# Optimization experiments

Hardware: AMD Instinct MI355X
Metric: run time of the kernel (lower is better)

## Reference

```python
import jax, jax.numpy as jnp
from jax import lax
import numpy as np

B, T, F = 64, 128, 16
H = 512
S = 2  # num_seg; SEG_DICT['2'] = [8, 6], seg_cumsum = [2, 10, 16]


def timestep_embedding(t, dim, max_period=10000.0):
    half = dim // 2
    freqs = jnp.exp(-jnp.log(max_period) * jnp.arange(half, dtype=jnp.float32) / half)
    args = t[:, None] * freqs  # [N, half]
    return jnp.concatenate([jnp.cos(args), jnp.sin(args)], axis=-1)  # [N, dim]


def setup_inputs() -> dict:
    key = jax.random.key(0)
    ks = jax.random.split(key, 16)
    sc = lambda *sh: 1.0 / np.sqrt(sh[-1])
    inp = {
        'x': jax.random.normal(ks[0], (B, T, F), dtype=jnp.float32),
        'lengths': jax.random.randint(ks[1], (B,), 1, T + 1),
        'h0': jax.random.uniform(ks[2], (B, H), dtype=jnp.float32),
        'c0': jax.random.uniform(ks[3], (B, H), dtype=jnp.float32),
        'W_is0': jax.random.normal(ks[4], (H, 8), dtype=jnp.float32) * sc(8),
        'b_is0': jax.random.normal(ks[5], (H,), dtype=jnp.float32) * 0.01,
        'W_is1': jax.random.normal(ks[6], (H, 6), dtype=jnp.float32) * sc(6),
        'b_is1': jax.random.normal(ks[7], (H,), dtype=jnp.float32) * 0.01,
        'W_ih': jax.random.normal(ks[8], (4 * H, 3 * H), dtype=jnp.float32) * sc(3 * H),
        'W_hh': jax.random.normal(ks[9], (4 * H, H), dtype=jnp.float32) * sc(H),
        'b_ih': jax.random.normal(ks[10], (4 * H,), dtype=jnp.float32) * 0.01,
        'b_hh': jax.random.normal(ks[11], (4 * H,), dtype=jnp.float32) * 0.01,
        'W_o': jax.random.normal(ks[12], (F - 2, S * H), dtype=jnp.float32) * sc(S * H),
        'b_o': jax.random.normal(ks[13], (F - 2,), dtype=jnp.float32) * 0.01,
    }
    return inp


def reference(x, lengths, h0, c0, W_is0, b_is0, W_is1, b_is1,
              W_ih, W_hh, b_ih, b_hh, W_o, b_o):
    b, t, f = x.shape
    h = h0.shape[1]
    xf = x.reshape(-1, f)  # [B*T, F]

    # timestep embeddings from the two time columns (learning_type='diff')
    tc = timestep_embedding(xf[:, 0], h)
    tp = timestep_embedding(xf[:, 1], h)
    t_emb = jnp.concatenate([tc, tp], axis=-1)  # [B*T, 2H]

    # per-segment input linears (segments = cols 2:10 and 10:16)
    e0 = xf[:, 2:10] @ W_is0.T + b_is0
    e1 = xf[:, 10:16] @ W_is1.T + b_is1
    e0 = jnp.concatenate([e0, t_emb], axis=-1)[:, None, :]  # [B*T, 1, 3H]
    e1 = jnp.concatenate([e1, t_emb], axis=-1)[:, None, :]
    # faithful to torch: concat on dim=1 then reshape(batch, num_seg, seq_len, -1)
    embs = jnp.concatenate([e0, e1], axis=1).reshape(b, S, t, 3 * h)

    def cell(carry, xt):
        hh, cc = carry
        gates = xt @ W_ih.T + b_ih + hh @ W_hh.T + b_hh
        i, fg, g, o = jnp.split(gates, 4, axis=-1)  # torch LSTMCell order i,f,g,o
        cc = jax.nn.sigmoid(fg) * cc + jax.nn.sigmoid(i) * jnp.tanh(g)
        hh = jax.nn.sigmoid(o) * jnp.tanh(cc)
        return (hh, cc), hh

    hs = []
    for s in range(S):  # shared cell weights across segments (same nn.LSTMCell object)
        xs = jnp.swapaxes(embs[:, s], 0, 1)  # [T, B, 3H]
        _, h_seq = lax.scan(cell, (h0, c0), xs)  # [T, B, H]
        hs.append(jnp.swapaxes(h_seq, 0, 1))  # [B, T, H]
    hidden_states = jnp.stack(hs, axis=-2)  # [B, T, S, H]; dropout rate 0 -> identity

    idx = lengths - 1  # final valid timestep per sequence
    hfin = hidden_states[jnp.arange(b), idx].reshape(b, S * h)  # [B, S*H]
    out = jax.nn.sigmoid(hfin @ W_o.T + b_o)  # mlp_o: Linear + Sigmoid
    return out
```

## Files before the change

### kernel.cpp

```cpp
#include <hip/hip_runtime.h>
#include <hip/hip_bf16.h>
#include <stdint.h>


typedef __attribute__((ext_vector_type(8))) short bf16x8_t;
typedef __attribute__((ext_vector_type(4))) float f32x4_t;

#define SENT 0xAAAAAAAAu

#define OFF_G      0u
#define OFF_TEMB   33554432u
#define OFF_HH     50331648u
#define OFF_WHH    67239936u
#define OFF_WMID   69337088u
#define OFF_WC0    73531392u
#define OFF_WC1    73596928u
#define OFF_BC     73662464u
#define OFF_HFIN   73678848u
#define OFF_GFLAG  73940992u

__device__ __forceinline__ float bf2f(uint16_t u){
  union { uint32_t i; float f; } v; v.i = ((uint32_t)u) << 16; return v.f;
}
__device__ __forceinline__ uint16_t f2b(float f){
  union { float f; uint32_t i; } v; v.f = f;
  uint32_t r = v.i + 0x7fffu + ((v.i >> 16) & 1u);
  return (uint16_t)(r >> 16);
}
__device__ __forceinline__ float sigm(float x){ return 1.0f/(1.0f + __expf(-x)); }
__device__ __forceinline__ float tanh_(float x){
  float xc = fminf(fmaxf(x, -15.f), 15.f);
  float t = __expf(2.f*xc);
  return (t - 1.f)/(t + 1.f);
}
__device__ __forceinline__ void gl_lds16(const void* g, void* l){
  __builtin_amdgcn_global_load_lds(
      (const __attribute__((address_space(1))) void*)g,
      (__attribute__((address_space(3))) void*)l, 16, 0, 0);
}

__global__ void prepAll(const float* __restrict__ x,
                        const float* __restrict__ W_ih, const float* __restrict__ W_hh,
                        const float* __restrict__ W_is0, const float* __restrict__ b_is0,
                        const float* __restrict__ W_is1, const float* __restrict__ b_is1,
                        const float* __restrict__ b_ih, const float* __restrict__ b_hh,
                        const float* __restrict__ h0,
                        uint16_t* __restrict__ whh_b, uint16_t* __restrict__ wmid_b,
                        float* __restrict__ wc0, float* __restrict__ wc1,
                        float* __restrict__ bc,
                        uint16_t* __restrict__ temb, uint16_t* __restrict__ h_hist,
                        uint32_t* __restrict__ gflag){
  const int bid = blockIdx.x, tid = threadIdx.x;
  if (bid < 2048){
    const int n = bid;
    __shared__ float wrow[512];
    __shared__ float red[16][17];
    wrow[tid]       = W_ih[(size_t)n*1536 + tid];
    wrow[tid + 256] = W_ih[(size_t)n*1536 + 256 + tid];
    for (int j = tid; j < 1024; j += 256)
      wmid_b[(size_t)n*1024 + j] = f2b(W_ih[(size_t)n*1536 + 512 + j]);
    for (int k = tid; k < 512; k += 256)
      whh_b[(size_t)n*512 + k] = f2b(W_hh[(size_t)n*512 + k]);
    __syncthreads();
    {
      const int d = tid >> 4, jp = tid & 15;
      float s = 0.f;
      const int kk0 = jp*32;
      if (d < 8){
        for (int k = kk0; k < kk0 + 32; ++k) s += wrow[k]*W_is0[k*8 + d];
      } else if (d < 14){
        int c = d - 8;
        for (int k = kk0; k < kk0 + 32; ++k) s += wrow[k]*W_is1[k*6 + c];
      } else if (d == 14){
        for (int k = kk0; k < kk0 + 32; ++k) s += wrow[k]*b_is0[k];
      } else {
        for (int k = kk0; k < kk0 + 32; ++k) s += wrow[k]*b_is1[k];
      }
      red[d][jp] = s;
    }
    __syncthreads();
    if (tid < 16){
      float tot = 0.f;
      #pragma unroll
      for (int i = 0; i < 16; ++i) tot += red[tid][i];
      if (tid < 8)        wc0[n*8 + tid] = tot;
      else if (tid < 14)  wc1[n*8 + (tid - 8)] = tot;
      else if (tid == 14) bc[n]        = b_ih[n] + b_hh[n] + tot;
      else                bc[2048 + n] = b_ih[n] + b_hh[n] + tot;
    } else if (tid == 16){
      wc1[n*8 + 6] = 0.f; wc1[n*8 + 7] = 0.f;
    }
  } else if (bid < 10240){
    const int rid = bid - 2048;
    const int k = tid;
    float x0 = x[(size_t)rid*16 + 0], x1 = x[(size_t)rid*16 + 1];
    float f = __expf((float)k * (-9.210340371976184f/256.f));
    float a0 = x0*f, a1 = x1*f;
    size_t base = (size_t)rid*1024;
    temb[base + k]        = f2b(__cosf(a0));
    temb[base + 256 + k]  = f2b(__sinf(a0));
    temb[base + 512 + k]  = f2b(__cosf(a1));
    temb[base + 768 + k]  = f2b(__sinf(a1));
  } else if (bid < 10368){
    int i = (bid - 10240)*256 + tid;
    uint32_t* hh = (uint32_t*)h_hist;
    int e    = i*2;
    int rrcg = e >> 9;
    int rr   = rrcg >> 4, cg = rrcg & 15;
    int rm   = e & 511;
    int row  = rm >> 5, u = rm & 31;
    int b    = (rr*16 + row) & 63;
    int unit = cg*32 + u;
    uint32_t lo = f2b(h0[(size_t)b*512 + unit]);
    uint32_t hi = f2b(h0[(size_t)b*512 + unit + 1]);
    uint32_t wd = lo | (hi << 16);
    if (wd == SENT) wd ^= 1u;
    hh[i] = wd;
    if (i < 1024) gflag[i] = 0u;
  } else {
    uint32_t* hh = (uint32_t*)h_hist;
    size_t w0 = 32768u + ((size_t)(bid - 10368)*256 + tid)*8;
    uint4 s4 = make_uint4(SENT, SENT, SENT, SENT);
    *(uint4*)&hh[w0]     = s4;
    *(uint4*)&hh[w0 + 4] = s4;
  }
}

__launch_bounds__(256)
__global__ void fusedk(const float* __restrict__ x, const float* __restrict__ c0,
                       const int* __restrict__ lengths,
                       const uint16_t* __restrict__ whh_b, const uint16_t* __restrict__ temb,
                       const uint16_t* __restrict__ wmid,
                       const float* __restrict__ wc0, const float* __restrict__ wc1,
                       const float* __restrict__ bc,
                       uint16_t* __restrict__ G, uint16_t* __restrict__ h_hist,
                       uint32_t* __restrict__ gflag, float* __restrict__ hfin){
  __shared__ __align__(16) uint16_t smem_u[17664];
  const int tid = threadIdx.x;
  const int bid = blockIdx.x;
  const int w = tid >> 6, lane = tid & 63;
  const int q = lane >> 4, ln = lane & 15;

  if (bid >= 128){
    const int gb = bid - 128;
    const int idx = gb >> 4;
    const int mt = (idx & 1) ? (idx >> 1) : (32 + (idx >> 1));
    const int n0 = (gb & 15)*128;
    uint16_t* Al = smem_u;
    uint16_t* Bl = smem_u + 8192;
    const int wm = w >> 1, wn = w & 1;
    const int srow_l = lane >> 3;
    const int scol = (((lane & 7) ^ srow_l)) * 8;

    f32x4_t acc[4][4];
    #pragma unroll
    for (int a = 0; a < 4; ++a)
      #pragma unroll
      for (int b2 = 0; b2 < 4; ++b2) acc[a][b2] = (f32x4_t){0.f,0.f,0.f,0.f};

    for (int kb = 0; kb < 16; ++kb){
      #pragma unroll
      for (int i = 0; i < 4; ++i){
        int row0 = w*32 + i*8;
        int lrow = row0 + srow_l;
        int bA = lrow & 63, ntmA = mt*2 + (lrow >> 6);
        gl_lds16(temb + (size_t)(bA*128 + ntmA)*1024 + kb*64 + scol, &Al[row0*64]);
        gl_lds16(wmid + (size_t)(n0 + lrow)*1024 + kb*64 + scol, &Bl[row0*64]);
      }
      __syncthreads();
      #pragma unroll
      for (int kc = 0; kc < 2; ++kc){
        const int sl = ((((kc << 2) | q) ^ (ln & 7)) << 3);
        bf16x8_t af[4], bf[4];
        #pragma unroll
        for (int mt_i = 0; mt_i < 4; ++mt_i)
          af[mt_i] = *(const bf16x8_t*)&Al[(wm*64 + mt_i*16 + ln)*64 + sl];
        #pragma unroll
        for (int nt = 0; nt < 4; ++nt)
          bf[nt] = *(const bf16x8_t*)&Bl[(wn*64 + nt*16 + ln)*64 + sl];
        #pragma unroll
        for (int mt_i = 0; mt_i < 4; ++mt_i)
          #pragma unroll
          for (int nt = 0; nt < 4; ++nt)
            acc[mt_i][nt] = __builtin_amdgcn_mfma_f32_16x16x32_bf16(af[mt_i], bf[nt], acc[mt_i][nt], 0, 0, 0);
      }
      __syncthreads();
    }
    #pragma unroll
    for (int mt_i = 0; mt_i < 4; ++mt_i)
      #pragma unroll
      for (int nt = 0; nt < 4; ++nt)
        #pragma unroll
        for (int r = 0; r < 4; ++r){
          int Mr = wm*64 + mt_i*16 + q*4 + r;
          int Nc = wn*64 + nt*16 + ln;
          smem_u[Mr*132 + Nc] = f2b(acc[mt_i][nt][r]);
        }
    __syncthreads();
    {
      const int erow = tid >> 1, eh = tid & 1;
      const unsigned long long* lsrc = (const unsigned long long*)&smem_u[erow*132 + eh*64];
      unsigned long long* gdst = (unsigned long long*)
          (G + (size_t)(mt*128 + erow)*2048 + n0 + eh*64);
      #pragma unroll
      for (int i2 = 0; i2 < 16; ++i2)
        __hip_atomic_store(&gdst[i2], lsrc[i2], __ATOMIC_RELAXED, __HIP_MEMORY_SCOPE_AGENT);
    }
    __syncthreads();
    if (tid == 0)
      __hip_atomic_store(&gflag[mt*16 + (gb & 15)], 1u,
                         __ATOMIC_RELEASE, __HIP_MEMORY_SCOPE_AGENT);
    return;
  }

  #define HL(b,r,c) smem_u[(((b)*16 + (r))*552) + (c)]
  const int rr = bid & 7;
  const int g  = bid >> 3;
  const int k0 = g*32;
  const int sp = rr >> 2;
  const int u8 = ln & 7, gh = ln >> 3;
  const int unit = k0 + w*8 + u8;
  const int gl0 = gh*512 + unit;
  const int gl1 = (2 + gh)*512 + unit;
  const int LVL = 65536;

  bf16x8_t barr0[16], barr1[16];
  #pragma unroll
  for (int kc = 0; kc < 16; ++kc){
    barr0[kc] = *(const bf16x8_t*)(whh_b + (size_t)gl0*512 + kc*32 + q*8);
    barr1[kc] = *(const bf16x8_t*)(whh_b + (size_t)gl1*512 + kc*32 + q*8);
  }
  bf16x8_t e0f[2], e1f[2];
  #pragma unroll
  for (int nsI = 0; nsI < 2; ++nsI){
    bf16x8_t v0 = {0,0,0,0,0,0,0,0}, v1 = {0,0,0,0,0,0,0,0};
    if (q == 0){
      const float* wcs = nsI ? wc1 : wc0;
      #pragma unroll
      for (int jj = 0; jj < 8; ++jj){
        ((uint16_t*)&v0)[jj] = f2b(wcs[gl0*8 + jj]);
        ((uint16_t*)&v1)[jj] = f2b(wcs[gl1*8 + jj]);
      }
    }
    e0f[nsI] = v0; e1f[nsI] = v1;
  }
  float bc0v[2] = { bc[gl0], bc[2048 + gl0] };
  float bc1v[2] = { bc[gl1], bc[2048 + gl1] };

  int   bmr[4], lenr[4];
  float cst[4];
  #pragma unroll
  for (int r = 0; r < 4; ++r){
    int row = rr*16 + q*4 + r;
    bmr[r]  = row & 63;
    lenr[r] = lengths[bmr[r]];
    cst[r]  = c0[(size_t)bmr[r]*512 + unit];
  }

  const int prow = lane >> 2;
  const int pcol = (lane & 3)*8;
  const int xm = tid >> 3, xc = tid & 7;
  const int xb = (rr*16 + xm) & 63;
  const size_t stb = ((size_t)rr*8192 + g*512);

  for (int idx2 = tid; idx2 < 2*16*32; idx2 += 256)
    HL(idx2 >> 9, (idx2 >> 5) & 15, 520 + (idx2 & 31)) = 0;

  uint32_t fl[4];
  {
    const uint32_t* gf0 = gflag + (sp*32)*16 + (g >> 2);
    #pragma unroll
    for (int j = 0; j < 4; ++j)
      fl[j] = __hip_atomic_load(&gf0[j*4], __ATOMIC_RELAXED, __HIP_MEMORY_SCOPE_AGENT);
  }

  for (int t = 0; t < 128; ++t){
    const int qidx = sp*128 + t;
    const int ntm = qidx >> 1;
    const int ns  = qidx & 1;
    const int buf = t & 1;

    if ((t & 3) == 0){
      const int mt = qidx >> 2;
      bool ok = (fl[0] != 0u) & (fl[1] != 0u) & (fl[2] != 0u) & (fl[3] != 0u);
      if (!ok){
        const uint32_t* gf = gflag + mt*16 + (g >> 2);
        while (true){
          ok = true;
          #pragma unroll
          for (int j = 0; j < 4; ++j){
            uint32_t v = __hip_atomic_load(&gf[j*4], __ATOMIC_RELAXED, __HIP_MEMORY_SCOPE_AGENT);
            ok &= (v != 0u);
          }
          if (ok) break;
          __builtin_amdgcn_s_sleep(1);
        }
      }
      if (t < 124){
        const uint32_t* gfn = gflag + (mt + 1)*16 + (g >> 2);
        #pragma unroll
        for (int j = 0; j < 4; ++j)
          fl[j] = __hip_atomic_load(&gfn[j*4], __ATOMIC_RELAXED, __HIP_MEMORY_SCOPE_AGENT);
      }
    }

    uint16_t g0r[4], g1r[4];
    #pragma unroll
    for (int r = 0; r < 4; ++r){
      size_t grow = (size_t)(ntm*64 + bmr[r])*2048;
      g0r[r] = G[grow + gl0];
      g1r[r] = G[grow + gl1];
    }
    float xv = 0.f;
    if (tid < 128){
      if (ns == 0)      xv = x[(size_t)(xb*128 + ntm)*16 + 2 + xc];
      else if (xc < 6)  xv = x[(size_t)(xb*128 + ntm)*16 + 10 + xc];
    }

    {
      const unsigned long long* lvl = (const unsigned long long*)h_hist
                                      + (((size_t)t*LVL + (size_t)rr*8192) >> 2);
      unsigned long long hv[4][2];
      while (true){
        bool ok = true;
        #pragma unroll
        for (int i = 0; i < 4; ++i){
          const unsigned long long* p = lvl + ((size_t)(w*4 + i)*128 + prow*8 + (pcol >> 2));
          hv[i][0] = __hip_atomic_load(&p[0], __ATOMIC_RELAXED, __HIP_MEMORY_SCOPE_AGENT);
          hv[i][1] = __hip_atomic_load(&p[1], __ATOMIC_RELAXED, __HIP_MEMORY_SCOPE_AGENT);
          ok &= ((uint32_t)hv[i][0] != SENT) & ((uint32_t)(hv[i][0] >> 32) != SENT)
              & ((uint32_t)hv[i][1] != SENT) & ((uint32_t)(hv[i][1] >> 32) != SENT);
        }
        if (__all(ok)) break;
      }
      #pragma unroll
      for (int i = 0; i < 4; ++i){
        int reg = w*4 + i;
        *(unsigned long long*)&HL(buf, prow, reg*32 + pcol)     = hv[i][0];
        *(unsigned long long*)&HL(buf, prow, reg*32 + pcol + 4) = hv[i][1];
      }
    }
    if (tid < 128) HL(buf, xm, 512 + xc) = f2b(xv);
    __syncthreads();

    f32x4_t acc0, acc1;
    {
      float b0 = ns ? bc0v[1] : bc0v[0];
      float b1 = ns ? bc1v[1] : bc1v[0];
      #pragma unroll
      for (int r = 0; r < 4; ++r){ acc0[r] = bf2f(g0r[r]) + b0; acc1[r] = bf2f(g1r[r]) + b1; }
    }
    #pragma unroll
    for (int kc = 0; kc < 16; ++kc){
      bf16x8_t a = *(const bf16x8_t*)&HL(buf, ln, kc*32 + q*8);
      acc0 = __builtin_amdgcn_mfma_f32_16x16x32_bf16(a, barr0[kc], acc0, 0, 0, 0);
      acc1 = __builtin_amdgcn_mfma_f32_16x16x32_bf16(a, barr1[kc], acc1, 0, 0, 0);
    }
    {
      bf16x8_t a = *(const bf16x8_t*)&HL(buf, ln, 512 + q*8);
      acc0 = __builtin_amdgcn_mfma_f32_16x16x32_bf16(a, ns ? e0f[1] : e0f[0], acc0, 0, 0, 0);
      acc1 = __builtin_amdgcn_mfma_f32_16x16x32_bf16(a, ns ? e1f[1] : e1f[0], acc1, 0, 0, 0);
    }

    float pf[4], po[4];
    #pragma unroll
    for (int r = 0; r < 4; ++r){
      pf[r] = __shfl_xor(acc0[r], 8);
      po[r] = __shfl_xor(acc1[r], 8);
    }
    if (ln < 8){
      uint32_t hb[4]; float hF[4];
      #pragma unroll
      for (int r = 0; r < 4; ++r){
        float ig = acc0[r], fg = pf[r], gg = acc1[r], og = po[r];
        cst[r] = sigm(fg)*cst[r] + sigm(ig)*tanh_(gg);
        float h = sigm(og)*tanh_(cst[r]);
        hF[r] = h; hb[r] = (uint32_t)f2b(h);
      }
      #pragma unroll
      for (int r = 0; r < 4; ++r){
        uint32_t ph = (uint32_t)__shfl_xor((int)hb[r], 1);
        uint32_t packed = hb[r] | (ph << 16);
        if (packed == SENT) packed ^= 1u;
        uint32_t hi = (uint32_t)__shfl_xor((int)packed, 2);
        if ((ln & 3) == 0){
          unsigned long long v = (unsigned long long)packed | ((unsigned long long)hi << 32);
          unsigned long long* hp = (unsigned long long*)h_hist
              + (((size_t)(t+1)*LVL + stb + (size_t)(q*4 + r)*32 + w*8 + u8) >> 2);
          __hip_atomic_store(hp, v, __ATOMIC_RELAXED, __HIP_MEMORY_SCOPE_AGENT);
        }
        if (t == lenr[r] - 1)
          hfin[(size_t)bmr[r]*1024 + sp*512 + unit] = hF[r];
      }
    }
  }
  #undef HL
}

__global__ void outk(const float* __restrict__ hfin, const float* __restrict__ W_o,
                     const float* __restrict__ b_o, float* __restrict__ out){
  __shared__ float hl[1024];
  __shared__ float red[16][17];
  const int b = blockIdx.x, tid = threadIdx.x;
  #pragma unroll
  for (int i = 0; i < 4; ++i) hl[tid + i*256] = hfin[(size_t)b*1024 + tid + i*256];
  __syncthreads();
  const int o = tid >> 4, j0 = tid & 15;
  float s = 0.f;
  if (o < 14){
    for (int j = j0; j < 1024; j += 16) s += hl[j]*W_o[(size_t)o*1024 + j];
  }
  red[o][j0] = s;
  __syncthreads();
  if (tid < 14){
    float tot = b_o[tid];
    #pragma unroll
    for (int i = 0; i < 16; ++i) tot += red[tid][i];
    out[b*14 + tid] = 1.0f/(1.0f + __expf(-tot));
  }
}

extern "C" void kernel_launch(void* const* d_in, const int* in_sizes, int n_in,
                              void* d_out, int out_size, void* d_ws, size_t ws_size,
                              hipStream_t stream){
  const float* x     = (const float*)d_in[0];
  const int*   lens  = (const int*)  d_in[1];
  const float* h0    = (const float*)d_in[2];
  const float* c0    = (const float*)d_in[3];
  const float* W_is0 = (const float*)d_in[4];
  const float* b_is0 = (const float*)d_in[5];
  const float* W_is1 = (const float*)d_in[6];
  const float* b_is1 = (const float*)d_in[7];
  const float* W_ih  = (const float*)d_in[8];
  const float* W_hh  = (const float*)d_in[9];
  const float* b_ih  = (const float*)d_in[10];
  const float* b_hh  = (const float*)d_in[11];
  const float* W_o   = (const float*)d_in[12];
  const float* b_o   = (const float*)d_in[13];
  float* out = (float*)d_out;

  char* ws = (char*)d_ws;
  uint16_t* G      = (uint16_t*)(ws + OFF_G);
  uint16_t* temb   = (uint16_t*)(ws + OFF_TEMB);
  uint16_t* h_hist = (uint16_t*)(ws + OFF_HH);
  uint16_t* whh_b  = (uint16_t*)(ws + OFF_WHH);
  uint16_t* wmid_b = (uint16_t*)(ws + OFF_WMID);
  float* wc0  = (float*)(ws + OFF_WC0);
  float* wc1  = (float*)(ws + OFF_WC1);
  float* bc   = (float*)(ws + OFF_BC);
  float* hfin = (float*)(ws + OFF_HFIN);
  uint32_t* gflag = (uint32_t*)(ws + OFF_GFLAG);

  hipLaunchKernelGGL(prepAll, dim3(12416), dim3(256), 0, stream,
                     x, W_ih, W_hh, W_is0, b_is0, W_is1, b_is1, b_ih, b_hh, h0,
                     whh_b, wmid_b, wc0, wc1, bc, temb, h_hist, gflag);
  hipLaunchKernelGGL(fusedk, dim3(1152), dim3(256), 0, stream,
                     x, c0, lens, whh_b, temb, wmid_b, wc0, wc1, bc,
                     G, h_hist, gflag, hfin);
  hipLaunchKernelGGL(outk, dim3(64), dim3(256), 0, stream, hfin, W_o, b_o, out);
}
```

Before: 558.3 us.

## Load recurrent h fragments directly into registers, drop LDS staging and barrier

Measured after the change: 846.6 us. +51.6%, slower.

```diff
diff --git a/kernel.cpp b/kernel.cpp
--- a/kernel.cpp
+++ b/kernel.cpp
@@ -5,6 +5,7 @@
 
 typedef __attribute__((ext_vector_type(8))) short bf16x8_t;
 typedef __attribute__((ext_vector_type(4))) float f32x4_t;
+typedef __attribute__((ext_vector_type(4))) unsigned int u32x4_t;
 
 #define SENT 0xAAAAAAAAu
 
@@ -38,6 +39,10 @@
       (const __attribute__((address_space(1))) void*)g,
       (__attribute__((address_space(3))) void*)l, 16, 0, 0);
 }
+
+#define LDREG(d, p, off) \
+  asm volatile("global_load_dwordx4 %0, %1, off offset:" #off " sc0 sc1" \
+               : "=v"(d) : "v"(p) : "memory")
 
 __global__ void prepAll(const float* __restrict__ x,
                         const float* __restrict__ W_ih, const float* __restrict__ W_hh,
@@ -213,7 +218,6 @@
     return;
   }
 
-  #define HL(b,r,c) smem_u[(((b)*16 + (r))*552) + (c)]
   const int rr = bid & 7;
   const int g  = bid >> 3;
   const int k0 = g*32;
@@ -257,14 +261,8 @@
     cst[r]  = c0[(size_t)bmr[r]*512 + unit];
   }
 
-  const int prow = lane >> 2;
-  const int pcol = (lane & 3)*8;
-  const int xm = tid >> 3, xc = tid & 7;
-  const int xb = (rr*16 + xm) & 63;
+  const int xbv = (rr*16 + ln) & 63;
   const size_t stb = ((size_t)rr*8192 + g*512);
-
-  for (int idx2 = tid; idx2 < 2*16*32; idx2 += 256)
-    HL(idx2 >> 9, (idx2 >> 5) & 15, 520 + (idx2 & 31)) = 0;
 
   uint32_t fl[4];
   {
@@ -278,7 +276,6 @@
     const int qidx = sp*128 + t;
     const int ntm = qidx >> 1;
     const int ns  = qidx & 1;
-    const int buf = t & 1;
 
     if ((t & 3) == 0){
       const int mt = qidx >> 2;
@@ -311,37 +308,60 @@
       g0r[r] = G[grow + gl0];
       g1r[r] = G[grow + gl1];
     }
-    float xv = 0.f;
-    if (tid < 128){
-      if (ns == 0)      xv = x[(size_t)(xb*128 + ntm)*16 + 2 + xc];
-      else if (xc < 6)  xv = x[(size_t)(xb*128 + ntm)*16 + 10 + xc];
-    }
-
+    bf16x8_t axf = (bf16x8_t){0,0,0,0,0,0,0,0};
+    if (q == 0){
+      const float2* xp2 = (const float2*)(x + ((size_t)xbv*128 + ntm)*16 + (ns ? 10 : 2));
+      float2 f0 = xp2[0], f1 = xp2[1], f2v = xp2[2];
+      uint16_t* ax = (uint16_t*)&axf;
+      ax[0] = f2b(f0.x); ax[1] = f2b(f0.y);
+      ax[2] = f2b(f1.x); ax[3] = f2b(f1.y);
+      ax[4] = f2b(f2v.x); ax[5] = f2b(f2v.y);
+      if (!ns){ float2 f3 = xp2[3]; ax[6] = f2b(f3.x); ax[7] = f2b(f3.y); }
+    }
+
+    u32x4_t fr[16];
     {
-      const unsigned long long* lvl = (const unsigned long long*)h_hist
-                                      + (((size_t)t*LVL + (size_t)rr*8192) >> 2);
-      unsigned long long hv[4][2];
+      const uint16_t* hb = h_hist + (size_t)t*LVL + (size_t)rr*8192 + ln*32 + q*8;
+      const uint16_t* pb0 = hb;
+      const uint16_t* pb1 = hb + 2048;
+      const uint16_t* pb2 = hb + 4096;
+      const uint16_t* pb3 = hb + 6144;
+      LDREG(fr[ 0], pb0, 0);    LDREG(fr[ 1], pb0, 1024);
+      LDREG(fr[ 2], pb0, 2048); LDREG(fr[ 3], pb0, 3072);
+      LDREG(fr[ 4], pb1, 0);    LDREG(fr[ 5], pb1, 1024);
+      LDREG(fr[ 6], pb1, 2048); LDREG(fr[ 7], pb1, 3072);
+      LDREG(fr[ 8], pb2, 0);    LDREG(fr[ 9], pb2, 1024);
+      LDREG(fr[10], pb2, 2048); LDREG(fr[11], pb2, 3072);
+      LDREG(fr[12], pb3, 0);    LDREG(fr[13], pb3, 1024);
+      LDREG(fr[14], pb3, 2048); LDREG(fr[15], pb3, 3072);
       while (true){
-        bool ok = true;
-        #pragma unroll
-        for (int i = 0; i < 4; ++i){
-          const unsigned long long* p = lvl + ((size_t)(w*4 + i)*128 + prow*8 + (pcol >> 2));
-          hv[i][0] = __hip_atomic_load(&p[0], __ATOMIC_RELAXED, __HIP_MEMORY_SCOPE_AGENT);
-          hv[i][1] = __hip_atomic_load(&p[1], __ATOMIC_RELAXED, __HIP_MEMORY_SCOPE_AGENT);
-          ok &= ((uint32_t)hv[i][0] != SENT) & ((uint32_t)(hv[i][0] >> 32) != SENT)
-              & ((uint32_t)hv[i][1] != SENT) & ((uint32_t)(hv[i][1] >> 32) != SENT);
-        }
-        if (__all(ok)) break;
-      }
-      #pragma unroll
-      for (int i = 0; i < 4; ++i){
-        int reg = w*4 + i;
-        *(unsigned long long*)&HL(buf, prow, reg*32 + pcol)     = hv[i][0];
-        *(unsigned long long*)&HL(buf, prow, reg*32 + pcol + 4) = hv[i][1];
-      }
-    }
-    if (tid < 128) HL(buf, xm, 512 + xc) = f2b(xv);
-    __syncthreads();
+        asm volatile("s_waitcnt vmcnt(0)" ::: "memory");
+        __builtin_amdgcn_sched_barrier(0);
+        unsigned stale = 0u;
+        #define CHK1(i) { if (fr[i][0]==SENT || fr[i][1]==SENT || fr[i][2]==SENT || fr[i][3]==SENT) stale |= (1u<<(i)); }
+        CHK1(0) CHK1(1) CHK1(2) CHK1(3) CHK1(4) CHK1(5) CHK1(6) CHK1(7)
+        CHK1(8) CHK1(9) CHK1(10) CHK1(11) CHK1(12) CHK1(13) CHK1(14) CHK1(15)
+        #undef CHK1
+        if (__all(stale == 0u)) break;
+        if (stale & (1u<< 0)) LDREG(fr[ 0], pb0, 0);
+        if (stale & (1u<< 1)) LDREG(fr[ 1], pb0, 1024);
+        if (stale & (1u<< 2)) LDREG(fr[ 2], pb0, 2048);
+        if (stale & (1u<< 3)) LDREG(fr[ 3], pb0, 3072);
+        if (stale & (1u<< 4)) LDREG(fr[ 4], pb1, 0);
+        if (stale & (1u<< 5)) LDREG(fr[ 5], pb1, 1024);
+        if (stale & (1u<< 6)) LDREG(fr[ 6], pb1, 2048);
+        if (stale & (1u<< 7)) LDREG(fr[ 7], pb1, 3072);
+        if (stale & (1u<< 8)) LDREG(fr[ 8], pb2, 0);
+        if (stale & (1u<< 9)) LDREG(fr[ 9], pb2, 1024);
+        if (stale & (1u<<10)) LDREG(fr[10], pb2, 2048);
+        if (stale & (1u<<11)) LDREG(fr[11], pb2, 3072);
+        if (stale & (1u<<12)) LDREG(fr[12], pb3, 0);
+        if (stale & (1u<<13)) LDREG(fr[13], pb3, 1024);
+        if (stale & (1u<<14)) LDREG(fr[14], pb3, 2048);
+        if (stale & (1u<<15)) LDREG(fr[15], pb3, 3072);
+      }
+      __builtin_amdgcn_sched_barrier(0);
+    }
 
     f32x4_t acc0, acc1;
     {
@@ -352,15 +372,12 @@
     }
     #pragma unroll
     for (int kc = 0; kc < 16; ++kc){
-      bf16x8_t a = *(const bf16x8_t*)&HL(buf, ln, kc*32 + q*8);
+      bf16x8_t a = *(const bf16x8_t*)&fr[kc];
       acc0 = __builtin_amdgcn_mfma_f32_16x16x32_bf16(a, barr0[kc], acc0, 0, 0, 0);
       acc1 = __builtin_amdgcn_mfma_f32_16x16x32_bf16(a, barr1[kc], acc1, 0, 0, 0);
     }
-    {
-      bf16x8_t a = *(const bf16x8_t*)&HL(buf, ln, 512 + q*8);
-      acc0 = __builtin_amdgcn_mfma_f32_16x16x32_bf16(a, ns ? e0f[1] : e0f[0], acc0, 0, 0, 0);
-      acc1 = __builtin_amdgcn_mfma_f32_16x16x32_bf16(a, ns ? e1f[1] : e1f[0], acc1, 0, 0, 0);
-    }
+    acc0 = __builtin_amdgcn_mfma_f32_16x16x32_bf16(axf, ns ? e0f[1] : e0f[0], acc0, 0, 0, 0);
+    acc1 = __builtin_amdgcn_mfma_f32_16x16x32_bf16(axf, ns ? e1f[1] : e1f[0], acc1, 0, 0, 0);
 
     float pf[4], po[4];
     #pragma unroll
@@ -369,18 +386,18 @@
       po[r] = __shfl_xor(acc1[r], 8);
     }
     if (ln < 8){
-      uint32_t hb[4]; float hF[4];
+      uint32_t hb2[4]; float hF[4];
       #pragma unroll
       for (int r = 0; r < 4; ++r){
         float ig = acc0[r], fg = pf[r], gg = acc1[r], og = po[r];
         cst[r] = sigm(fg)*cst[r] + sigm(ig)*tanh_(gg);
         float h = sigm(og)*tanh_(cst[r]);
-        hF[r] = h; hb[r] = (uint32_t)f2b(h);
+        hF[r] = h; hb2[r] = (uint32_t)f2b(h);
       }
       #pragma unroll
       for (int r = 0; r < 4; ++r){
-        uint32_t ph = (uint32_t)__shfl_xor((int)hb[r], 1);
-        uint32_t packed = hb[r] | (ph << 16);
+        uint32_t ph = (uint32_t)__shfl_xor((int)hb2[r], 1);
+        uint32_t packed = hb2[r] | (ph << 16);
         if (packed == SENT) packed ^= 1u;
         uint32_t hi = (uint32_t)__shfl_xor((int)packed, 2);
         if ((ln & 3) == 0){
@@ -394,7 +411,6 @@
       }
     }
   }
-  #undef HL
 }
 
 __global__ void outk(const float* __restrict__ hfin, const float* __restrict__ W_o,
```

## Pipeline h polling loads and start own-chunk MFMAs before block barrier

Applied to the files above, without the earlier changes.

Measured after the change: 1.008 ms. 80.6% more time.

```diff
diff --git a/kernel.cpp b/kernel.cpp
--- a/kernel.cpp
+++ b/kernel.cpp
@@ -317,31 +317,49 @@
       else if (xc < 6)  xv = x[(size_t)(xb*128 + ntm)*16 + 10 + xc];
     }
 
+    unsigned long long hvA[4][2], hvB[4][2];
     {
       const unsigned long long* lvl = (const unsigned long long*)h_hist
                                       + (((size_t)t*LVL + (size_t)rr*8192) >> 2);
-      unsigned long long hv[4][2];
+      const unsigned long long* p0 = lvl + ((size_t)(w*4)*128 + prow*8 + (pcol >> 2));
+      #define LOAD8(hv) { \
+        hv[0][0] = __hip_atomic_load(&p0[  0], __ATOMIC_RELAXED, __HIP_MEMORY_SCOPE_AGENT); \
+        hv[0][1] = __hip_atomic_load(&p0[  1], __ATOMIC_RELAXED, __HIP_MEMORY_SCOPE_AGENT); \
+        hv[1][0] = __hip_atomic_load(&p0[128], __ATOMIC_RELAXED, __HIP_MEMORY_SCOPE_AGENT); \
+        hv[1][1] = __hip_atomic_load(&p0[129], __ATOMIC_RELAXED, __HIP_MEMORY_SCOPE_AGENT); \
+        hv[2][0] = __hip_atomic_load(&p0[256], __ATOMIC_RELAXED, __HIP_MEMORY_SCOPE_AGENT); \
+        hv[2][1] = __hip_atomic_load(&p0[257], __ATOMIC_RELAXED, __HIP_MEMORY_SCOPE_AGENT); \
+        hv[3][0] = __hip_atomic_load(&p0[384], __ATOMIC_RELAXED, __HIP_MEMORY_SCOPE_AGENT); \
+        hv[3][1] = __hip_atomic_load(&p0[385], __ATOMIC_RELAXED, __HIP_MEMORY_SCOPE_AGENT); }
+      #define CHKOK(hv) ( ((uint32_t)hv[0][0] != SENT) & ((uint32_t)(hv[0][0] >> 32) != SENT) \
+                        & ((uint32_t)hv[0][1] != SENT) & ((uint32_t)(hv[0][1] >> 32) != SENT) \
+                        & ((uint32_t)hv[1][0] != SENT) & ((uint32_t)(hv[1][0] >> 32) != SENT) \
+                        & ((uint32_t)hv[1][1] != SENT) & ((uint32_t)(hv[1][1] >> 32) != SENT) \
+                        & ((uint32_t)hv[2][0] != SENT) & ((uint32_t)(hv[2][0] >> 32) != SENT) \
+                        & ((uint32_t)hv[2][1] != SENT) & ((uint32_t)(hv[2][1] >> 32) != SENT) \
+                        & ((uint32_t)hv[3][0] != SENT) & ((uint32_t)(hv[3][0] >> 32) != SENT) \
+                        & ((uint32_t)hv[3][1] != SENT) & ((uint32_t)(hv[3][1] >> 32) != SENT) )
+      LOAD8(hvA);
       while (true){
-        bool ok = true;
-        #pragma unroll
-        for (int i = 0; i < 4; ++i){
-          const unsigned long long* p = lvl + ((size_t)(w*4 + i)*128 + prow*8 + (pcol >> 2));
-          hv[i][0] = __hip_atomic_load(&p[0], __ATOMIC_RELAXED, __HIP_MEMORY_SCOPE_AGENT);
-          hv[i][1] = __hip_atomic_load(&p[1], __ATOMIC_RELAXED, __HIP_MEMORY_SCOPE_AGENT);
-          ok &= ((uint32_t)hv[i][0] != SENT) & ((uint32_t)(hv[i][0] >> 32) != SENT)
-              & ((uint32_t)hv[i][1] != SENT) & ((uint32_t)(hv[i][1] >> 32) != SENT);
+        LOAD8(hvB);
+        if (__all(CHKOK(hvA))) break;
+        LOAD8(hvA);
+        if (__all(CHKOK(hvB))){
+          #pragma unroll
+          for (int i = 0; i < 4; ++i){ hvA[i][0] = hvB[i][0]; hvA[i][1] = hvB[i][1]; }
+          break;
         }
-        if (__all(ok)) break;
-      }
-      #pragma unroll
-      for (int i = 0; i < 4; ++i){
-        int reg = w*4 + i;
-        *(unsigned long long*)&HL(buf, prow, reg*32 + pcol)     = hv[i][0];
-        *(unsigned long long*)&HL(buf, prow, reg*32 + pcol + 4) = hv[i][1];
-      }
+      }
+      #undef LOAD8
+      #undef CHKOK
+    }
+    #pragma unroll
+    for (int i = 0; i < 4; ++i){
+      int reg = w*4 + i;
+      *(unsigned long long*)&HL(buf, prow, reg*32 + pcol)     = hvA[i][0];
+      *(unsigned long long*)&HL(buf, prow, reg*32 + pcol + 4) = hvA[i][1];
     }
     if (tid < 128) HL(buf, xm, 512 + xc) = f2b(xv);
-    __syncthreads();
 
     f32x4_t acc0, acc1;
     {
@@ -351,10 +369,23 @@
       for (int r = 0; r < 4; ++r){ acc0[r] = bf2f(g0r[r]) + b0; acc1[r] = bf2f(g1r[r]) + b1; }
     }
     #pragma unroll
-    for (int kc = 0; kc < 16; ++kc){
+    for (int i = 0; i < 4; ++i){
+      int kc = w*4 + i;
       bf16x8_t a = *(const bf16x8_t*)&HL(buf, ln, kc*32 + q*8);
       acc0 = __builtin_amdgcn_mfma_f32_16x16x32_bf16(a, barr0[kc], acc0, 0, 0, 0);
       acc1 = __builtin_amdgcn_mfma_f32_16x16x32_bf16(a, barr1[kc], acc1, 0, 0, 0);
+    }
+    __syncthreads();
+    #pragma unroll
+    for (int j = 1; j < 4; ++j){
+      int wo = ((w + j) & 3)*4;
+      #pragma unroll
+      for (int i = 0; i < 4; ++i){
+        int kc = wo + i;
+        bf16x8_t a = *(const bf16x8_t*)&HL(buf, ln, kc*32 + q*8);
+        acc0 = __builtin_amdgcn_mfma_f32_16x16x32_bf16(a, barr0[kc], acc0, 0, 0, 0);
+        acc1 = __builtin_amdgcn_mfma_f32_16x16x32_bf16(a, barr1[kc], acc1, 0, 0, 0);
+      }
     }
     {
       bf16x8_t a = *(const bf16x8_t*)&HL(buf, ln, 512 + q*8);
```
